# Kernel tuning notes

Measured on AMD Instinct MI355X. Metric: run time of the kernel, lower is better.

Reference implementation:

```python
import jax, jax.numpy as jnp
import numpy as np

DROPOUT_P = 0.5
INV_SCALE = 1.0
_DROP_KEY = jax.random.key(42)


def setup_inputs() -> dict:
    key = jax.random.key(0)
    kq, kk, kv = jax.random.split(key, 3)
    B, H, S, D = 4, 16, 2048, 64
    return {
        "query": jax.random.normal(kq, (B, H, S, D), dtype=jnp.float32),
        "key": jax.random.normal(kk, (B, H, S, D), dtype=jnp.float32),
        "value": jax.random.normal(kv, (B, H, S, D), dtype=jnp.float32),
    }


def reference(query, key, value):
    # qk = Q @ K^T, scaled, softmax over last axis
    qk = jnp.einsum("bhqd,bhkd->bhqk", query, key) / INV_SCALE
    p = jax.nn.softmax(qk, axis=-1)
    # inverted dropout with a fixed RNG key (deterministic reference)
    keep = jax.random.bernoulli(_DROP_KEY, 1.0 - DROPOUT_P, p.shape)
    p = jnp.where(keep, p / (1.0 - DROPOUT_P), 0.0)
    # attention output: P @ V
    return jnp.einsum("bhqk,bhkd->bhqd", p, value)
```

## Files before the change

kernel.cpp:

```cpp
#include <hip/hip_runtime.h>


#define S_LEN 2048
#define D_DIM 64
#define KT    32
#define QT    16
#define NWAVE 4
#define KSTR  72
#define VROW  66
#define PSTR  40

typedef short  short8  __attribute__((ext_vector_type(8)));
typedef float  floatx4 __attribute__((ext_vector_type(4)));

#define TF_R2(sh) \
  "v_add_u32 %1, %1, %0\n\t" \
  "v_add_u32 %3, %3, %2\n\t" \
  "v_alignbit_b32 %0, %0, %0, " #sh "\n\t" \
  "v_alignbit_b32 %2, %2, %2, " #sh "\n\t" \
  "v_xor_b32 %0, %0, %1\n\t" \
  "v_xor_b32 %2, %2, %3\n\t"

__device__ __forceinline__ void tf2(unsigned i0, unsigned i1,
                                    unsigned& w0, unsigned& w1) {
  unsigned a0, a1;
  asm(
    "v_add_u32 %0, 42, %4\n\t"
    "v_add_u32 %2, 42, %5\n\t"
    "v_mov_b32 %1, %0\n\t"
    "v_mov_b32 %3, %2\n\t"
    "v_alignbit_b32 %0, %0, %0, 19\n\t"
    "v_alignbit_b32 %2, %2, %2, 19\n\t"
    "v_xor_b32 %0, %0, %1\n\t"
    "v_xor_b32 %2, %2, %3\n\t"
    TF_R2(17) TF_R2(6) TF_R2(26)
    "v_add_u32 %1, 42, %1\n\t"
    "v_add_u32 %3, 42, %3\n\t"
    "v_add_u32 %0, 0x1bd11bf1, %0\n\t"
    "v_add_u32 %2, 0x1bd11bf1, %2\n\t"
    TF_R2(15) TF_R2(3) TF_R2(16) TF_R2(8)
    "v_add_u32 %1, 0x1bd11bf0, %1\n\t"
    "v_add_u32 %3, 0x1bd11bf0, %3\n\t"
    "v_add_u32 %0, 2, %0\n\t"
    "v_add_u32 %2, 2, %2\n\t"
    TF_R2(19) TF_R2(17) TF_R2(6) TF_R2(26)
    "v_add_u32 %0, 45, %0\n\t"
    "v_add_u32 %2, 45, %2\n\t"
    TF_R2(15) TF_R2(3) TF_R2(16) TF_R2(8)
    "v_add_u32 %1, 42, %1\n\t"
    "v_add_u32 %3, 42, %3\n\t"
    "v_add_u32 %0, 0x1bd11bf4, %0\n\t"
    "v_add_u32 %2, 0x1bd11bf4, %2\n\t"
    TF_R2(19) TF_R2(17) TF_R2(6) TF_R2(26)
    "v_add_u32 %1, 0x1bd11bf0, %1\n\t"
    "v_add_u32 %3, 0x1bd11bf0, %3\n\t"
    "v_add_u32 %0, 5, %0\n\t"
    "v_add_u32 %2, 5, %2\n\t"
    "v_xor_b32 %0, %0, %1\n\t"
    "v_xor_b32 %2, %2, %3"
    : "=&v"(w0), "=&v"(a0), "=&v"(w1), "=&v"(a1)
    : "v"(i0), "v"(i1));
}

__device__ __forceinline__ void split_bf16(float x, unsigned short& h, unsigned short& l) {
  unsigned u = __float_as_uint(x);
  h = (unsigned short)(u >> 16);
  float r = x - __uint_as_float(u & 0xFFFF0000u);
  l = (unsigned short)(__float_as_uint(r) >> 16);
}

#define MFMA(a, b, c) __builtin_amdgcn_mfma_f32_16x16x32_bf16((a), (b), (c), 0, 0, 0)

__global__ __launch_bounds__(256, 6) void attn_fused_v10(
    const float* __restrict__ Qg, const float* __restrict__ Kg,
    const float* __restrict__ Vg, float* __restrict__ Og) {

  __shared__ __attribute__((aligned(16))) unsigned short Kh[KT * KSTR];
  __shared__ __attribute__((aligned(16))) unsigned short Kl[KT * KSTR];
  __shared__ __attribute__((aligned(16))) unsigned short Vs[KT * VROW];
  __shared__ __attribute__((aligned(16))) unsigned short Ph[NWAVE][QT * PSTR];

  const int tid  = threadIdx.x;
  const int wave = tid >> 6;
  const int lane = tid & 63;
  const int m16  = lane & 15;
  const int quad = lane >> 4;

  const int bh    = blockIdx.x >> 5;
  const int qtile = blockIdx.x & 31;
  const int q0    = qtile * (QT * NWAVE) + wave * QT;
  const size_t head_off = (size_t)bh * S_LEN * D_DIM;

  short8 qh[2], ql[2];
#pragma unroll
  for (int kc = 0; kc < 2; ++kc) {
    const float* qp = Qg + head_off + (size_t)(q0 + m16) * D_DIM + kc * 32 + quad * 8;
    floatx4 f0 = *(const floatx4*)qp;
    floatx4 f1 = *(const floatx4*)(qp + 4);
#pragma unroll
    for (int e = 0; e < 4; ++e) {
      unsigned short h, l;
      split_bf16(f0[e], h, l);
      qh[kc][e] = (short)h;  ql[kc][e] = (short)l;
      split_bf16(f1[e], h, l);
      qh[kc][4 + e] = (short)h;  ql[kc][4 + e] = (short)l;
    }
  }

  floatx4 o_acc[4];
#pragma unroll
  for (int n = 0; n < 4; ++n) o_acc[n] = (floatx4){0.f, 0.f, 0.f, 0.f};
  float lsum[4];
#pragma unroll
  for (int r = 0; r < 4; ++r) lsum[r] = 0.f;

  const unsigned ibase0 =
      ((unsigned)(bh * S_LEN + q0 + quad * 4)) * (unsigned)S_LEN + (unsigned)m16;

  for (int kb = 0; kb < S_LEN; kb += KT) {
    __syncthreads();

    for (int f = tid; f < KT * (D_DIM / 4); f += 256) {
      int row = f >> 4;
      int c4  = (f & 15) << 2;
      size_t goff = head_off + (size_t)(kb + row) * D_DIM + c4;
      floatx4 kv = *(const floatx4*)(Kg + goff);
      floatx4 vv = *(const floatx4*)(Vg + goff);
      unsigned short h0, h1, h2, h3, l0, l1, l2, l3;
      split_bf16(kv[0], h0, l0); split_bf16(kv[1], h1, l1);
      split_bf16(kv[2], h2, l2); split_bf16(kv[3], h3, l3);
      int kidx = row * KSTR + c4;
      *(unsigned*)&Kh[kidx]     = (unsigned)h0 | ((unsigned)h1 << 16);
      *(unsigned*)&Kh[kidx + 2] = (unsigned)h2 | ((unsigned)h3 << 16);
      *(unsigned*)&Kl[kidx]     = (unsigned)l0 | ((unsigned)l1 << 16);
      *(unsigned*)&Kl[kidx + 2] = (unsigned)l2 | ((unsigned)l3 << 16);
      unsigned v01 = (__float_as_uint(vv[0]) >> 16) |
                     (__float_as_uint(vv[1]) & 0xFFFF0000u);
      unsigned v23 = (__float_as_uint(vv[2]) >> 16) |
                     (__float_as_uint(vv[3]) & 0xFFFF0000u);
      int vidx = row * VROW + c4;
      *(unsigned*)&Vs[vidx]     = v01;
      *(unsigned*)&Vs[vidx + 2] = v23;
    }
    __syncthreads();

    floatx4 sc[2];
#pragma unroll
    for (int nb = 0; nb < 2; ++nb) {
      floatx4 acc = (floatx4){0.f, 0.f, 0.f, 0.f};
#pragma unroll
      for (int kc = 0; kc < 2; ++kc) {
        int bidx = (nb * 16 + m16) * KSTR + kc * 32 + quad * 8;
        short8 kbh = *(const short8*)&Kh[bidx];
        short8 kbl = *(const short8*)&Kl[bidx];
        acc = MFMA(qh[kc], kbh, acc);
        acc = MFMA(qh[kc], kbl, acc);
        acc = MFMA(ql[kc], kbh, acc);
      }
      sc[nb] = acc;
    }

#pragma unroll
    for (int r = 0; r < 4; ++r) {
      unsigned i0 = ibase0 + (unsigned)kb + (unsigned)(r * S_LEN);
      unsigned w0, w1;
      tf2(i0, i0 + 16u, w0, w1);
#pragma unroll
      for (int nb = 0; nb < 2; ++nb) {
        float pe = __expf(sc[nb][r]);
        lsum[r] += pe;
        unsigned hbits = __float_as_uint(pe) >> 16;
        unsigned w = nb ? w1 : w0;
        hbits = ((int)w < 0) ? 0u : hbits;
        Ph[wave][(quad * 4 + r) * PSTR + nb * 16 + m16] = (unsigned short)hbits;
      }
    }

    short8 pa = *(const short8*)&Ph[wave][m16 * PSTR + quad * 8];
#pragma unroll
    for (int n = 0; n < 4; ++n) {
      short8 vb;
#pragma unroll
      for (int j = 0; j < 8; ++j)
        vb[j] = (short)Vs[(quad * 8 + j) * VROW + n * 16 + m16];
      o_acc[n] = MFMA(pa, vb, o_acc[n]);
    }
  }

#pragma unroll
  for (int off = 8; off >= 1; off >>= 1)
#pragma unroll
    for (int r = 0; r < 4; ++r)
      lsum[r] += __shfl_xor(lsum[r], off, 64);

#pragma unroll
  for (int r = 0; r < 4; ++r) {
    float scale = 2.0f / lsum[r];
#pragma unroll
    for (int n = 0; n < 4; ++n) {
      Og[head_off + (size_t)(q0 + quad * 4 + r) * D_DIM + n * 16 + m16] =
          o_acc[n][r] * scale;
    }
  }
}

extern "C" void kernel_launch(void* const* d_in, const int* in_sizes, int n_in,
                              void* d_out, int out_size, void* d_ws, size_t ws_size,
                              hipStream_t stream) {
  (void)in_sizes; (void)n_in; (void)out_size; (void)d_ws; (void)ws_size;
  const float* Q = (const float*)d_in[0];
  const float* K = (const float*)d_in[1];
  const float* V = (const float*)d_in[2];
  float* O = (float*)d_out;
  hipLaunchKernelGGL(attn_fused_v10, dim3(2048), dim3(256), 0, stream, Q, K, V, O);
}
```

Baseline: 799.7 us.

## Pre-split K into bf16 hi/lo planes in workspace via a separate prep kernel

Adds a prep kernel that converts K once into bf16 high and low arrays in the workspace. The attention kernel then copies pre-split K tiles straight into LDS instead of re-splitting fp32 K in every block, which happens 32 times per head. It also hoists the LDS pointer arithmetic out of the inner loop. The trade is an extra launch plus an extra global write and read of the split K, and the path only runs when the workspace is large enough.

```diff
diff --git a/kernel.cpp b/kernel.cpp
--- a/kernel.cpp
+++ b/kernel.cpp
@@ -12,6 +12,7 @@
 
 typedef short  short8  __attribute__((ext_vector_type(8)));
 typedef float  floatx4 __attribute__((ext_vector_type(4)));
+typedef unsigned uint2v __attribute__((ext_vector_type(2)));
 
 #define TF_R2(sh) \
   "v_add_u32 %1, %1, %0\n\t" \
@@ -71,9 +72,30 @@
 
 #define MFMA(a, b, c) __builtin_amdgcn_mfma_f32_16x16x32_bf16((a), (b), (c), 0, 0, 0)
 
-__global__ __launch_bounds__(256, 6) void attn_fused_v10(
+__global__ __launch_bounds__(256) void prep_kv(
+    const float* __restrict__ Kg, unsigned short* __restrict__ KHg,
+    unsigned short* __restrict__ KLg) {
+  unsigned t  = blockIdx.x * 256u + threadIdx.x;
+  unsigned i4 = t * 4u;
+  floatx4 kv = *(const floatx4*)(Kg + i4);
+  unsigned short h0, h1, h2, h3, l0, l1, l2, l3;
+  split_bf16(kv[0], h0, l0); split_bf16(kv[1], h1, l1);
+  split_bf16(kv[2], h2, l2); split_bf16(kv[3], h3, l3);
+  uint2v hh, ll;
+  hh[0] = (unsigned)h0 | ((unsigned)h1 << 16);
+  hh[1] = (unsigned)h2 | ((unsigned)h3 << 16);
+  ll[0] = (unsigned)l0 | ((unsigned)l1 << 16);
+  ll[1] = (unsigned)l2 | ((unsigned)l3 << 16);
+  *(uint2v*)(KHg + i4) = hh;
+  *(uint2v*)(KLg + i4) = ll;
+}
+
+template <bool PREPPED>
+__global__ __launch_bounds__(256, 6) void attn_v11(
     const float* __restrict__ Qg, const float* __restrict__ Kg,
-    const float* __restrict__ Vg, float* __restrict__ Og) {
+    const float* __restrict__ Vg, float* __restrict__ Og,
+    const unsigned short* __restrict__ KHg,
+    const unsigned short* __restrict__ KLg) {
 
   __shared__ __attribute__((aligned(16))) unsigned short Kh[KT * KSTR];
   __shared__ __attribute__((aligned(16))) unsigned short Kl[KT * KSTR];
@@ -117,30 +139,58 @@
   const unsigned ibase0 =
       ((unsigned)(bh * S_LEN + q0 + quad * 4)) * (unsigned)S_LEN + (unsigned)m16;
 
+  const unsigned short* kh_rd = &Kh[m16 * KSTR + quad * 8];
+  const unsigned short* kl_rd = &Kl[m16 * KSTR + quad * 8];
+  const unsigned short* v_rd  = &Vs[(quad * 8) * VROW + m16];
+  unsigned short*       p_wr  = &Ph[wave][(quad * 4) * PSTR + m16];
+  const unsigned short* p_rd  = &Ph[wave][m16 * PSTR + quad * 8];
+
   for (int kb = 0; kb < S_LEN; kb += KT) {
     __syncthreads();
 
-    for (int f = tid; f < KT * (D_DIM / 4); f += 256) {
-      int row = f >> 4;
-      int c4  = (f & 15) << 2;
-      size_t goff = head_off + (size_t)(kb + row) * D_DIM + c4;
-      floatx4 kv = *(const floatx4*)(Kg + goff);
-      floatx4 vv = *(const floatx4*)(Vg + goff);
-      unsigned short h0, h1, h2, h3, l0, l1, l2, l3;
-      split_bf16(kv[0], h0, l0); split_bf16(kv[1], h1, l1);
-      split_bf16(kv[2], h2, l2); split_bf16(kv[3], h3, l3);
-      int kidx = row * KSTR + c4;
-      *(unsigned*)&Kh[kidx]     = (unsigned)h0 | ((unsigned)h1 << 16);
-      *(unsigned*)&Kh[kidx + 2] = (unsigned)h2 | ((unsigned)h3 << 16);
-      *(unsigned*)&Kl[kidx]     = (unsigned)l0 | ((unsigned)l1 << 16);
-      *(unsigned*)&Kl[kidx + 2] = (unsigned)l2 | ((unsigned)l3 << 16);
-      unsigned v01 = (__float_as_uint(vv[0]) >> 16) |
-                     (__float_as_uint(vv[1]) & 0xFFFF0000u);
-      unsigned v23 = (__float_as_uint(vv[2]) >> 16) |
-                     (__float_as_uint(vv[3]) & 0xFFFF0000u);
-      int vidx = row * VROW + c4;
-      *(unsigned*)&Vs[vidx]     = v01;
-      *(unsigned*)&Vs[vidx + 2] = v23;
+    if constexpr (PREPPED) {
+      const int row = tid >> 3;
+      const int c8  = (tid & 7) * 8;
+      const size_t koff = head_off + (size_t)(kb + row) * D_DIM + c8;
+      short8 kh8 = *(const short8*)(KHg + koff);
+      short8 kl8 = *(const short8*)(KLg + koff);
+      *(short8*)&Kh[row * KSTR + c8] = kh8;
+      *(short8*)&Kl[row * KSTR + c8] = kl8;
+      for (int f = tid; f < KT * (D_DIM / 4); f += 256) {
+        int vrow = f >> 4;
+        int c4   = (f & 15) << 2;
+        floatx4 vv = *(const floatx4*)(Vg + head_off + (size_t)(kb + vrow) * D_DIM + c4);
+        unsigned v01 = (__float_as_uint(vv[0]) >> 16) |
+                       (__float_as_uint(vv[1]) & 0xFFFF0000u);
+        unsigned v23 = (__float_as_uint(vv[2]) >> 16) |
+                       (__float_as_uint(vv[3]) & 0xFFFF0000u);
+        int vidx = vrow * VROW + c4;
+        *(unsigned*)&Vs[vidx]     = v01;
+        *(unsigned*)&Vs[vidx + 2] = v23;
+      }
+    } else {
+      for (int f = tid; f < KT * (D_DIM / 4); f += 256) {
+        int row = f >> 4;
+        int c4  = (f & 15) << 2;
+        size_t goff = head_off + (size_t)(kb + row) * D_DIM + c4;
+        floatx4 kv = *(const floatx4*)(Kg + goff);
+        floatx4 vv = *(const floatx4*)(Vg + goff);
+        unsigned short h0, h1, h2, h3, l0, l1, l2, l3;
+        split_bf16(kv[0], h0, l0); split_bf16(kv[1], h1, l1);
+        split_bf16(kv[2], h2, l2); split_bf16(kv[3], h3, l3);
+        int kidx = row * KSTR + c4;
+        *(unsigned*)&Kh[kidx]     = (unsigned)h0 | ((unsigned)h1 << 16);
+        *(unsigned*)&Kh[kidx + 2] = (unsigned)h2 | ((unsigned)h3 << 16);
+        *(unsigned*)&Kl[kidx]     = (unsigned)l0 | ((unsigned)l1 << 16);
+        *(unsigned*)&Kl[kidx + 2] = (unsigned)l2 | ((unsigned)l3 << 16);
+        unsigned v01 = (__float_as_uint(vv[0]) >> 16) |
+                       (__float_as_uint(vv[1]) & 0xFFFF0000u);
+        unsigned v23 = (__float_as_uint(vv[2]) >> 16) |
+                       (__float_as_uint(vv[3]) & 0xFFFF0000u);
+        int vidx = row * VROW + c4;
+        *(unsigned*)&Vs[vidx]     = v01;
+        *(unsigned*)&Vs[vidx + 2] = v23;
+      }
     }
     __syncthreads();
 
@@ -150,9 +200,8 @@
       floatx4 acc = (floatx4){0.f, 0.f, 0.f, 0.f};
 #pragma unroll
       for (int kc = 0; kc < 2; ++kc) {
-        int bidx = (nb * 16 + m16) * KSTR + kc * 32 + quad * 8;
-        short8 kbh = *(const short8*)&Kh[bidx];
-        short8 kbl = *(const short8*)&Kl[bidx];
+        short8 kbh = *(const short8*)&kh_rd[nb * 16 * KSTR + kc * 32];
+        short8 kbl = *(const short8*)&kl_rd[nb * 16 * KSTR + kc * 32];
         acc = MFMA(qh[kc], kbh, acc);
         acc = MFMA(qh[kc], kbl, acc);
         acc = MFMA(ql[kc], kbh, acc);
@@ -172,17 +221,17 @@
         unsigned hbits = __float_as_uint(pe) >> 16;
         unsigned w = nb ? w1 : w0;
         hbits = ((int)w < 0) ? 0u : hbits;
-        Ph[wave][(quad * 4 + r) * PSTR + nb * 16 + m16] = (unsigned short)hbits;
-      }
-    }
-
-    short8 pa = *(const short8*)&Ph[wave][m16 * PSTR + quad * 8];
+        p_wr[r * PSTR + nb * 16] = (unsigned short)hbits;
+      }
+    }
+
+    short8 pa = *(const short8*)p_rd;
 #pragma unroll
     for (int n = 0; n < 4; ++n) {
       short8 vb;
 #pragma unroll
       for (int j = 0; j < 8; ++j)
-        vb[j] = (short)Vs[(quad * 8 + j) * VROW + n * 16 + m16];
+        vb[j] = (short)v_rd[j * VROW + n * 16];
       o_acc[n] = MFMA(pa, vb, o_acc[n]);
     }
   }
@@ -207,10 +256,24 @@
 extern "C" void kernel_launch(void* const* d_in, const int* in_sizes, int n_in,
                               void* d_out, int out_size, void* d_ws, size_t ws_size,
                               hipStream_t stream) {
-  (void)in_sizes; (void)n_in; (void)out_size; (void)d_ws; (void)ws_size;
+  (void)in_sizes; (void)n_in; (void)out_size;
   const float* Q = (const float*)d_in[0];
   const float* K = (const float*)d_in[1];
   const float* V = (const float*)d_in[2];
   float* O = (float*)d_out;
-  hipLaunchKernelGGL(attn_fused_v10, dim3(2048), dim3(256), 0, stream, Q, K, V, O);
-}
+
+  const size_t KELTS = (size_t)64 * S_LEN * D_DIM;
+  const size_t NEED  = 2 * KELTS * sizeof(unsigned short);
+  if (d_ws != nullptr && ws_size >= NEED) {
+    unsigned short* KH = (unsigned short*)d_ws;
+    unsigned short* KL = KH + KELTS;
+    hipLaunchKernelGGL(prep_kv, dim3((unsigned)(KELTS / 4 / 256)), dim3(256),
+                       0, stream, K, KH, KL);
+    hipLaunchKernelGGL((attn_v11<true>), dim3(2048), dim3(256), 0, stream,
+                       Q, K, V, O, KH, KL);
+  } else {
+    hipLaunchKernelGGL((attn_v11<false>), dim3(2048), dim3(256), 0, stream,
+                       Q, K, V, O, (const unsigned short*)nullptr,
+                       (const unsigned short*)nullptr);
+  }
+}
```

Measured after the change: 766.9 us. 4.1% less time.

## Precompute bf16 K split and transposed V in workspace, drop LDS staging

Applied to the files above, without the earlier changes.

Adds two pre-pass kernels. One splits K into bf16 hi/lo arrays and the other writes a tile-transposed bf16 V, both into the workspace buffer. The attention kernel then loads MFMA operand fragments straight from global memory, with no LDS staging of K/V and no block-wide barriers per tile, and with occupancy hint 4. The cost is extra launches and a round trip of the precomputed arrays through global memory, and the old fused kernel is kept as a fallback when the workspace is too small.

```diff
diff --git a/kernel.cpp b/kernel.cpp
--- a/kernel.cpp
+++ b/kernel.cpp
@@ -12,6 +12,7 @@
 
 typedef short  short8  __attribute__((ext_vector_type(8)));
 typedef float  floatx4 __attribute__((ext_vector_type(4)));
+typedef unsigned uint2v __attribute__((ext_vector_type(2)));
 
 #define TF_R2(sh) \
   "v_add_u32 %1, %1, %0\n\t" \
@@ -71,13 +72,53 @@
 
 #define MFMA(a, b, c) __builtin_amdgcn_mfma_f32_16x16x32_bf16((a), (b), (c), 0, 0, 0)
 
-__global__ __launch_bounds__(256, 6) void attn_fused_v10(
-    const float* __restrict__ Qg, const float* __restrict__ Kg,
-    const float* __restrict__ Vg, float* __restrict__ Og) {
-
-  __shared__ __attribute__((aligned(16))) unsigned short Kh[KT * KSTR];
-  __shared__ __attribute__((aligned(16))) unsigned short Kl[KT * KSTR];
-  __shared__ __attribute__((aligned(16))) unsigned short Vs[KT * VROW];
+__global__ __launch_bounds__(256) void prep_k(
+    const float* __restrict__ Kg, unsigned short* __restrict__ KHg,
+    unsigned short* __restrict__ KLg) {
+  unsigned t  = blockIdx.x * 256u + threadIdx.x;
+  unsigned i4 = t * 4u;
+  floatx4 kv = *(const floatx4*)(Kg + i4);
+  unsigned short h0, h1, h2, h3, l0, l1, l2, l3;
+  split_bf16(kv[0], h0, l0); split_bf16(kv[1], h1, l1);
+  split_bf16(kv[2], h2, l2); split_bf16(kv[3], h3, l3);
+  uint2v hh, ll;
+  hh[0] = (unsigned)h0 | ((unsigned)h1 << 16);
+  hh[1] = (unsigned)h2 | ((unsigned)h3 << 16);
+  ll[0] = (unsigned)l0 | ((unsigned)l1 << 16);
+  ll[1] = (unsigned)l2 | ((unsigned)l3 << 16);
+  *(uint2v*)(KHg + i4) = hh;
+  *(uint2v*)(KLg + i4) = ll;
+}
+
+__global__ __launch_bounds__(256) void prep_vt(
+    const float* __restrict__ Vg, unsigned short* __restrict__ VTg) {
+  __shared__ unsigned short T[D_DIM][40];
+  const int bh   = blockIdx.x >> 6;
+  const int tile = blockIdx.x & 63;
+  const int tid  = threadIdx.x;
+  const int row  = tid >> 3;
+  const int c8   = (tid & 7) * 8;
+  const float* vp = Vg + (size_t)bh * S_LEN * D_DIM + (size_t)(tile * 32 + row) * D_DIM + c8;
+  floatx4 v0 = *(const floatx4*)vp;
+  floatx4 v1 = *(const floatx4*)(vp + 4);
+#pragma unroll
+  for (int e = 0; e < 4; ++e) {
+    T[c8 + e][row]     = (unsigned short)(__float_as_uint(v0[e]) >> 16);
+    T[c8 + 4 + e][row] = (unsigned short)(__float_as_uint(v1[e]) >> 16);
+  }
+  __syncthreads();
+  const int col = tid >> 2;
+  const int r0  = (tid & 3) * 8;
+  short8 out = *(const short8*)&T[col][r0];
+  *(short8*)(VTg + ((size_t)blockIdx.x * D_DIM) * 32 + (size_t)tid * 8) = out;
+}
+
+__global__ __launch_bounds__(256, 4) void attn_v13(
+    const float* __restrict__ Qg, float* __restrict__ Og,
+    const unsigned short* __restrict__ KHg,
+    const unsigned short* __restrict__ KLg,
+    const unsigned short* __restrict__ VTg) {
+
   __shared__ __attribute__((aligned(16))) unsigned short Ph[NWAVE][QT * PSTR];
 
   const int tid  = threadIdx.x;
@@ -117,9 +158,131 @@
   const unsigned ibase0 =
       ((unsigned)(bh * S_LEN + q0 + quad * 4)) * (unsigned)S_LEN + (unsigned)m16;
 
+  const unsigned short* khp = KHg + head_off + (size_t)(m16 * D_DIM + quad * 8);
+  const unsigned short* klp = KLg + head_off + (size_t)(m16 * D_DIM + quad * 8);
+  const unsigned short* vtp = VTg + head_off + (size_t)(m16 * 32 + quad * 8);
+
+  unsigned short*       p_wr = &Ph[wave][(quad * 4) * PSTR + m16];
+  const unsigned short* p_rd = &Ph[wave][m16 * PSTR + quad * 8];
+
+  for (int kb = 0; kb < S_LEN; kb += KT) {
+    const unsigned short* kh_i = khp + (size_t)kb * D_DIM;
+    const unsigned short* kl_i = klp + (size_t)kb * D_DIM;
+    const unsigned short* vt_i = vtp + (size_t)(kb >> 5) * (D_DIM * 32);
+    short8 kfh[2][2], kfl[2][2], vf[4];
+#pragma unroll
+    for (int nb = 0; nb < 2; ++nb)
+#pragma unroll
+      for (int kc = 0; kc < 2; ++kc) {
+        kfh[nb][kc] = *(const short8*)(kh_i + nb * 16 * D_DIM + kc * 32);
+        kfl[nb][kc] = *(const short8*)(kl_i + nb * 16 * D_DIM + kc * 32);
+      }
+#pragma unroll
+    for (int n = 0; n < 4; ++n)
+      vf[n] = *(const short8*)(vt_i + n * 16 * 32);
+
+    unsigned w[8];
+#pragma unroll
+    for (int r = 0; r < 4; ++r) {
+      unsigned i0 = ibase0 + (unsigned)kb + (unsigned)(r * S_LEN);
+      tf2(i0, i0 + 16u, w[r * 2], w[r * 2 + 1]);
+    }
+
+    floatx4 sc[2];
+#pragma unroll
+    for (int nb = 0; nb < 2; ++nb) {
+      floatx4 acc = (floatx4){0.f, 0.f, 0.f, 0.f};
+#pragma unroll
+      for (int kc = 0; kc < 2; ++kc) {
+        acc = MFMA(qh[kc], kfh[nb][kc], acc);
+        acc = MFMA(qh[kc], kfl[nb][kc], acc);
+        acc = MFMA(ql[kc], kfh[nb][kc], acc);
+      }
+      sc[nb] = acc;
+    }
+
+#pragma unroll
+    for (int r = 0; r < 4; ++r)
+#pragma unroll
+      for (int nb = 0; nb < 2; ++nb) {
+        float pe = __expf(sc[nb][r]);
+        lsum[r] += pe;
+        unsigned hbits = __float_as_uint(pe) >> 16;
+        hbits = ((int)w[r * 2 + nb] < 0) ? 0u : hbits;
+        p_wr[r * PSTR + nb * 16] = (unsigned short)hbits;
+      }
+
+    short8 pa = *(const short8*)p_rd;
+#pragma unroll
+    for (int n = 0; n < 4; ++n)
+      o_acc[n] = MFMA(pa, vf[n], o_acc[n]);
+  }
+
+#pragma unroll
+  for (int off = 8; off >= 1; off >>= 1)
+#pragma unroll
+    for (int r = 0; r < 4; ++r)
+      lsum[r] += __shfl_xor(lsum[r], off, 64);
+
+#pragma unroll
+  for (int r = 0; r < 4; ++r) {
+    float scale = 2.0f / lsum[r];
+#pragma unroll
+    for (int n = 0; n < 4; ++n) {
+      Og[head_off + (size_t)(q0 + quad * 4 + r) * D_DIM + n * 16 + m16] =
+          o_acc[n][r] * scale;
+    }
+  }
+}
+
+__global__ __launch_bounds__(256, 6) void attn_mono(
+    const float* __restrict__ Qg, const float* __restrict__ Kg,
+    const float* __restrict__ Vg, float* __restrict__ Og) {
+
+  __shared__ __attribute__((aligned(16))) unsigned short Kh[KT * KSTR];
+  __shared__ __attribute__((aligned(16))) unsigned short Kl[KT * KSTR];
+  __shared__ __attribute__((aligned(16))) unsigned short Vs[KT * VROW];
+  __shared__ __attribute__((aligned(16))) unsigned short Ph[NWAVE][QT * PSTR];
+
+  const int tid  = threadIdx.x;
+  const int wave = tid >> 6;
+  const int lane = tid & 63;
+  const int m16  = lane & 15;
+  const int quad = lane >> 4;
+
+  const int bh    = blockIdx.x >> 5;
+  const int qtile = blockIdx.x & 31;
+  const int q0    = qtile * (QT * NWAVE) + wave * QT;
+  const size_t head_off = (size_t)bh * S_LEN * D_DIM;
+
+  short8 qh[2], ql[2];
+#pragma unroll
+  for (int kc = 0; kc < 2; ++kc) {
+    const float* qp = Qg + head_off + (size_t)(q0 + m16) * D_DIM + kc * 32 + quad * 8;
+    floatx4 f0 = *(const floatx4*)qp;
+    floatx4 f1 = *(const floatx4*)(qp + 4);
+#pragma unroll
+    for (int e = 0; e < 4; ++e) {
+      unsigned short h, l;
+      split_bf16(f0[e], h, l);
+      qh[kc][e] = (short)h;  ql[kc][e] = (short)l;
+      split_bf16(f1[e], h, l);
+      qh[kc][4 + e] = (short)h;  ql[kc][4 + e] = (short)l;
+    }
+  }
+
+  floatx4 o_acc[4];
+#pragma unroll
+  for (int n = 0; n < 4; ++n) o_acc[n] = (floatx4){0.f, 0.f, 0.f, 0.f};
+  float lsum[4];
+#pragma unroll
+  for (int r = 0; r < 4; ++r) lsum[r] = 0.f;
+
+  const unsigned ibase0 =
+      ((unsigned)(bh * S_LEN + q0 + quad * 4)) * (unsigned)S_LEN + (unsigned)m16;
+
   for (int kb = 0; kb < S_LEN; kb += KT) {
     __syncthreads();
-
     for (int f = tid; f < KT * (D_DIM / 4); f += 256) {
       int row = f >> 4;
       int c4  = (f & 15) << 2;
@@ -207,10 +370,23 @@
 extern "C" void kernel_launch(void* const* d_in, const int* in_sizes, int n_in,
                               void* d_out, int out_size, void* d_ws, size_t ws_size,
                               hipStream_t stream) {
-  (void)in_sizes; (void)n_in; (void)out_size; (void)d_ws; (void)ws_size;
+  (void)in_sizes; (void)n_in; (void)out_size;
   const float* Q = (const float*)d_in[0];
   const float* K = (const float*)d_in[1];
   const float* V = (const float*)d_in[2];
   float* O = (float*)d_out;
-  hipLaunchKernelGGL(attn_fused_v10, dim3(2048), dim3(256), 0, stream, Q, K, V, O);
-}
+
+  const size_t KELTS = (size_t)64 * S_LEN * D_DIM;
+  const size_t NEED  = 3 * KELTS * sizeof(unsigned short);
+  if (d_ws != nullptr && ws_size >= NEED) {
+    unsigned short* KH = (unsigned short*)d_ws;
+    unsigned short* KL = KH + KELTS;
+    unsigned short* VT = KL + KELTS;
+    hipLaunchKernelGGL(prep_k, dim3((unsigned)(KELTS / 4 / 256)), dim3(256),
+                       0, stream, K, KH, KL);
+    hipLaunchKernelGGL(prep_vt, dim3(64 * 64), dim3(256), 0, stream, V, VT);
+    hipLaunchKernelGGL(attn_v13, dim3(2048), dim3(256), 0, stream, Q, O, KH, KL, VT);
+  } else {
+    hipLaunchKernelGGL(attn_mono, dim3(2048), dim3(256), 0, stream, Q, K, V, O);
+  }
+}
```

Measured after the change: 744.6 us. -6.9%, faster.
